# Performance work log

Hardware: AMD Instinct MI355X
Metric: run time of the kernel (lower is better)

## Reference

```python
import jax, jax.numpy as jnp
import numpy as np
from jax import lax

BN_EPS = 1e-5


def _fps(xyz, n_points):
    """Farthest point sampling. xyz: [B,N,3] -> [B,S] int32 indices.
    Sequential by nature; expressed as a lax.scan over S iterations.
    Deterministic start at index 0 (original uses a random start)."""
    B, N, _ = xyz.shape

    def step(carry, _):
        distance, farthest = carry  # [B,N], [B]
        centroid = jax.vmap(lambda p, f: p[f])(xyz, farthest)  # [B,3]
        dist = jnp.sum((xyz - centroid[:, None, :]) ** 2, axis=-1)  # [B,N]
        distance = jnp.minimum(distance, dist)
        new_far = jnp.argmax(distance, axis=-1).astype(jnp.int32)
        return (distance, new_far), farthest

    init = (jnp.full((B, N), 1e10, xyz.dtype), jnp.zeros((B,), jnp.int32))
    _, idxs = lax.scan(step, init, None, length=n_points)  # [S,B]
    return idxs.T  # [B,S]


def _gather(points, idx):
    """index_points: points [B,N,C], idx [B,...] -> [B,...,C]."""
    return jax.vmap(lambda p, i: p[i])(points, idx)


def _conv_bn_relu(x, W, b, gamma, beta):
    # 1x1 Conv2d over channel axis: x [B,Cin,k,S] -> [B,Cout,k,S]
    y = jnp.einsum('oc,bcks->boks', W, x) + b[None, :, None, None]
    # BatchNorm2d in training mode: batch stats over (B,k,S), biased variance
    m = jnp.mean(y, axis=(0, 2, 3), keepdims=True)
    v = jnp.var(y, axis=(0, 2, 3), keepdims=True)
    y = (y - m) * lax.rsqrt(v + BN_EPS) * gamma[None, :, None, None] + beta[None, :, None, None]
    return jax.nn.relu(y)


def setup_inputs() -> dict:
    key = jax.random.key(0)
    ks = jax.random.split(key, 4)
    B, N, D = 4, 16384, 125
    C0, C1, C2 = 128, 128, 256  # C0 = 3 + D
    xyz = jax.random.normal(ks[0], (B, N, 3), jnp.float32)
    features = jax.random.normal(ks[1], (B, N, D), jnp.float32)
    W1 = jax.random.normal(ks[2], (C1, C0), jnp.float32) / np.float32(np.sqrt(C0))
    W2 = jax.random.normal(ks[3], (C2, C1), jnp.float32) / np.float32(np.sqrt(C1))
    return {
        'xyz': xyz, 'features': features,
        'W1': W1, 'b1': jnp.zeros((C1,), jnp.float32),
        'gamma1': jnp.ones((C1,), jnp.float32), 'beta1': jnp.zeros((C1,), jnp.float32),
        'W2': W2, 'b2': jnp.zeros((C2,), jnp.float32),
        'gamma2': jnp.ones((C2,), jnp.float32), 'beta2': jnp.zeros((C2,), jnp.float32),
        'n_points_fps': 2048, 'k': 16,
    }


def reference(xyz, features, W1, b1, gamma1, beta1, W2, b2, gamma2, beta2, n_points_fps, k):
    B, N, _ = xyz.shape
    S = n_points_fps
    # sample_and_group
    fps_idx = _fps(xyz, S)                     # [B,S]
    new_xyz = _gather(xyz, fps_idx)            # [B,S,3]
    # full pairwise squared distances [B,S,N] (as in square_distance)
    dists = jnp.sum((new_xyz[:, :, None, :] - xyz[:, None, :, :]) ** 2, axis=-1)
    _, idx = lax.top_k(-dists, k)              # k nearest, ascending distance: [B,S,k]
    grouped_xyz = _gather(xyz, idx)            # [B,S,k,3]
    grouped_xyz_norm = grouped_xyz - new_xyz[:, :, None, :]
    grouped_feat = _gather(features, idx)      # [B,S,k,D]
    new_points = jnp.concatenate([grouped_xyz_norm, grouped_feat], axis=-1)  # [B,S,k,C0]
    # MLP head: permute to [B,C0,k,S]
    x = jnp.transpose(new_points, (0, 3, 2, 1))
    x = _conv_bn_relu(x, W1, b1, gamma1, beta1)
    x = _conv_bn_relu(x, W2, b2, gamma2, beta2)
    x = jnp.max(x, axis=2)                     # max over neighbors k: [B,C2,S]
    x = jnp.transpose(x, (0, 2, 1))            # [B,S,C2]
    return (new_xyz, x)
```

## Files before the change

kernel.cpp:

```cpp
#include <hip/hip_runtime.h>

#define B_ 4
#define N_ 16384
#define D_ 125
#define S_ 2048
#define K_ 16
#define C0_ 128
#define C1_ 128
#define C2_ 256
#define NSLOT 64

typedef float v2f __attribute__((ext_vector_type(2)));

__device__ __forceinline__ void pin(float& x) { asm volatile("" : "+v"(x)); }

__device__ __forceinline__ v2f v2max(v2f a, v2f b) {
  v2f r;
  r.x = fmaxf(a.x, b.x);
  r.y = fmaxf(a.y, b.y);
  return r;
}

template <int CTRL, int RMASK>
__device__ __forceinline__ double dppmax(double k) {
  const long long kb = __double_as_longlong(k);
  const int lo = (int)(kb & 0xffffffffll);
  const int hi = (int)(((unsigned long long)kb) >> 32);
  const int plo = __builtin_amdgcn_update_dpp(lo, lo, CTRL, RMASK, 0xf, false);
  const int phi = __builtin_amdgcn_update_dpp(hi, hi, CTRL, RMASK, 0xf, false);
  const double p =
      __longlong_as_double(((long long)phi << 32) | (unsigned int)plo);
  return fmax(k, p);
}
template <int CTRL, int RMASK>
__device__ __forceinline__ double dppmin(double k) {
  const long long kb = __double_as_longlong(k);
  const int lo = (int)(kb & 0xffffffffll);
  const int hi = (int)(((unsigned long long)kb) >> 32);
  const int plo = __builtin_amdgcn_update_dpp(lo, lo, CTRL, RMASK, 0xf, false);
  const int phi = __builtin_amdgcn_update_dpp(hi, hi, CTRL, RMASK, 0xf, false);
  const double p =
      __longlong_as_double(((long long)phi << 32) | (unsigned int)plo);
  return fmin(k, p);
}

__global__ __attribute__((amdgpu_flat_work_group_size(1024, 1024),
                          amdgpu_waves_per_eu(4, 4)))
void fps_a_kernel(const float* __restrict__ xyz, float* __restrict__ new_xyz,
                  float* __restrict__ sortbuf, float* __restrict__ dsp,
                  float4* __restrict__ ccsp, unsigned int* __restrict__ invsp,
                  unsigned long long* __restrict__ klsp,
                  float4* __restrict__ csp) {
#pragma clang fp contract(off)
  const int b = blockIdx.x;
  const float* X = xyz + (size_t)b * N_ * 3;
  float* SB = sortbuf + (size_t)b * 3 * N_;
  const int t = threadIdx.x;
  constexpr int PAIRS = N_ / 1024 / 2;
  const int base = t * (2 * PAIRS);

  __shared__ unsigned int s_hist[4096];
  __shared__ float s_bb[16][8];
  __shared__ unsigned int s_wsum[16];
  __shared__ unsigned short s_sidx[N_];
  __shared__ unsigned long long s_k1[2];
  __shared__ __align__(16) float4 s_cc[2][16];

  float arr[48];
  {
    float4* a4 = (float4*)arr;
#pragma unroll
    for (int i = 0; i < 12; ++i) a4[i] = *(const float4*)(X + base * 3 + 4 * i);
  }
  float lx0 = arr[0], lx1 = arr[0], ly0 = arr[1], ly1 = arr[1];
  float lz0 = arr[2], lz1 = arr[2];
#pragma unroll
  for (int p = 1; p < 16; ++p) {
    lx0 = fminf(lx0, arr[3 * p + 0]); lx1 = fmaxf(lx1, arr[3 * p + 0]);
    ly0 = fminf(ly0, arr[3 * p + 1]); ly1 = fmaxf(ly1, arr[3 * p + 1]);
    lz0 = fminf(lz0, arr[3 * p + 2]); lz1 = fmaxf(lz1, arr[3 * p + 2]);
  }
#pragma unroll
  for (int off = 32; off > 0; off >>= 1) {
    lx0 = fminf(lx0, __shfl_xor(lx0, off)); lx1 = fmaxf(lx1, __shfl_xor(lx1, off));
    ly0 = fminf(ly0, __shfl_xor(ly0, off)); ly1 = fmaxf(ly1, __shfl_xor(ly1, off));
    lz0 = fminf(lz0, __shfl_xor(lz0, off)); lz1 = fmaxf(lz1, __shfl_xor(lz1, off));
  }
  if ((t & 63) == 0) {
    const int w = t >> 6;
    s_bb[w][0] = lx0; s_bb[w][1] = lx1; s_bb[w][2] = ly0;
    s_bb[w][3] = ly1; s_bb[w][4] = lz0; s_bb[w][5] = lz1;
  }
  for (int i = t; i < 4096; i += 1024) s_hist[i] = 0u;
  if (t == 0) { s_k1[0] = 0ull; s_k1[1] = 0ull; }
  __syncthreads();
  float gx0 = s_bb[0][0], gx1 = s_bb[0][1], gy0 = s_bb[0][2];
  float gy1 = s_bb[0][3], gz0 = s_bb[0][4], gz1 = s_bb[0][5];
#pragma unroll
  for (int w = 1; w < 16; ++w) {
    gx0 = fminf(gx0, s_bb[w][0]); gx1 = fmaxf(gx1, s_bb[w][1]);
    gy0 = fminf(gy0, s_bb[w][2]); gy1 = fmaxf(gy1, s_bb[w][3]);
    gz0 = fminf(gz0, s_bb[w][4]); gz1 = fmaxf(gz1, s_bb[w][5]);
  }
  const float ivx = (gx1 > gx0) ? 16.0f / (gx1 - gx0) : 0.0f;
  const float ivy = (gy1 > gy0) ? 16.0f / (gy1 - gy0) : 0.0f;
  const float ivz = (gz1 > gz0) ? 16.0f / (gz1 - gz0) : 0.0f;
  int cell[16];
#pragma unroll
  for (int p = 0; p < 16; ++p) {
    int qx = min(15, (int)((arr[3 * p + 0] - gx0) * ivx));
    int qy = min(15, (int)((arr[3 * p + 1] - gy0) * ivy));
    int qz = min(15, (int)((arr[3 * p + 2] - gz0) * ivz));
    int mx = (qx & 1) | ((qx & 2) << 2) | ((qx & 4) << 4) | ((qx & 8) << 6);
    int my = (qy & 1) | ((qy & 2) << 2) | ((qy & 4) << 4) | ((qy & 8) << 6);
    int mz = (qz & 1) | ((qz & 2) << 2) | ((qz & 4) << 4) | ((qz & 8) << 6);
    cell[p] = mx | (my << 1) | (mz << 2);
    atomicAdd(&s_hist[cell[p]], 1u);
  }
  __syncthreads();
  {
    unsigned int c0 = s_hist[4 * t + 0], c1 = s_hist[4 * t + 1];
    unsigned int c2 = s_hist[4 * t + 2], c3 = s_hist[4 * t + 3];
    (void)c3;
    unsigned int tsum = c0 + c1 + c2 + c3;
    unsigned int incl = tsum;
#pragma unroll
    for (int off = 1; off < 64; off <<= 1) {
      unsigned int nv = __shfl_up(incl, off);
      if ((t & 63) >= off) incl += nv;
    }
    if ((t & 63) == 63) s_wsum[t >> 6] = incl;
    __syncthreads();
    unsigned int wpre = 0;
    const int myw = t >> 6;
    for (int w = 0; w < myw; ++w) wpre += s_wsum[w];
    const unsigned int texc = wpre + incl - tsum;
    s_hist[4 * t + 0] = texc;
    s_hist[4 * t + 1] = texc + c0;
    s_hist[4 * t + 2] = texc + c0 + c1;
    s_hist[4 * t + 3] = texc + c0 + c1 + c2;
  }
  __syncthreads();
#pragma unroll
  for (int p = 0; p < 16; ++p) {
    const unsigned int slot = atomicAdd(&s_hist[cell[p]], 1u);
    SB[slot]          = arr[3 * p + 0];
    SB[N_ + slot]     = arr[3 * p + 1];
    SB[2 * N_ + slot] = arr[3 * p + 2];
    s_sidx[slot] = (unsigned short)(base + p);
  }
  __threadfence();
  __syncthreads();
  __threadfence();

  v2f px[PAIRS], py[PAIRS], pz[PAIRS], d[PAIRS];
  {
    float4 xa[4], ya[4], za[4];
#pragma unroll
    for (int i = 0; i < 4; ++i) {
      xa[i] = *(const float4*)(SB + base + 4 * i);
      ya[i] = *(const float4*)(SB + N_ + base + 4 * i);
      za[i] = *(const float4*)(SB + 2 * N_ + base + 4 * i);
    }
    const float* xf = (const float*)xa;
    const float* yf = (const float*)ya;
    const float* zf = (const float*)za;
#pragma unroll
    for (int j = 0; j < PAIRS; ++j) {
      px[j] = (v2f){xf[2 * j], xf[2 * j + 1]};
      py[j] = (v2f){yf[2 * j], yf[2 * j + 1]};
      pz[j] = (v2f){zf[2 * j], zf[2 * j + 1]};
      d[j] = (v2f){1e10f, 1e10f};
    }
  }
  unsigned int invw[PAIRS];
  {
    const unsigned int* SI = (const unsigned int*)&s_sidx[base];
#pragma unroll
    for (int j = 0; j < PAIRS; ++j) invw[j] = ~SI[j];
  }
  float bx0 = 1e30f, bx1 = -1e30f, by0 = 1e30f, by1 = -1e30f;
  float bz0 = 1e30f, bz1 = -1e30f;
#pragma unroll
  for (int j = 0; j < PAIRS; ++j) {
    bx0 = fminf(bx0, fminf(px[j].x, px[j].y));
    bx1 = fmaxf(bx1, fmaxf(px[j].x, px[j].y));
    by0 = fminf(by0, fminf(py[j].x, py[j].y));
    by1 = fmaxf(by1, fmaxf(py[j].x, py[j].y));
    bz0 = fminf(bz0, fminf(pz[j].x, pz[j].y));
    bz1 = fmaxf(bz1, fmaxf(pz[j].x, pz[j].y));
  }
#pragma unroll
  for (int j = 0; j < PAIRS; ++j) {
    float a0 = px[j].x, a1 = px[j].y;
    float b0 = py[j].x, b1 = py[j].y;
    float c0 = pz[j].x, c1 = pz[j].y;
    pin(a0); pin(a1); pin(b0); pin(b1); pin(c0); pin(c1);
    px[j] = (v2f){a0, a1};
    py[j] = (v2f){b0, b1};
    pz[j] = (v2f){c0, c1};
  }
  float cx = X[0], cy = X[1], cz = X[2];
  float tmax = 1e10f;
  unsigned long long keylow = 0ull;
  bool iwin = false;
  float ccx = 0.f, ccy = 0.f, ccz = 0.f;
  float cap_x = 0.f, cap_y = 0.f, cap_z = 0.f;
  const unsigned int wid = (unsigned int)(t >> 6);
  for (int s = 0; s < 1024; ++s) {
    if (((s - t) & 1023) == 0) { cap_x = cx; cap_y = cy; cap_z = cz; }
    if ((s & 1023) == 1023) {
      const int o = (b * S_ + (s & ~1023) + t) * 3;
      new_xyz[o + 0] = cap_x;
      new_xyz[o + 1] = cap_y;
      new_xyz[o + 2] = cap_z;
    }
    const int buf = s & 1;
    const float mx = fmaxf(fmaxf(bx0 - cx, cx - bx1), 0.0f);
    const float my = fmaxf(fmaxf(by0 - cy, cy - by1), 0.0f);
    const float mz = fmaxf(fmaxf(bz0 - cz, cz - bz1), 0.0f);
    const float L = (mx * mx + my * my) + mz * mz;
    if (__any(L < tmax)) {
      __builtin_amdgcn_s_setprio(1);
      const v2f c2x = {cx, cx}, c2y = {cy, cy}, c2z = {cz, cz};
#pragma unroll
      for (int j = 0; j < PAIRS; ++j) {
        v2f dx = px[j] - c2x;
        v2f dy = py[j] - c2y;
        v2f dz = pz[j] - c2z;
        v2f sq = (dx * dx + dy * dy) + dz * dz;
        v2f dm;
        dm.x = fminf(d[j].x, sq.x);
        dm.y = fminf(d[j].y, sq.y);
        d[j] = dm;
      }
      const v2f m01 = v2max(d[0], d[1]);
      const v2f m23 = v2max(d[2], d[3]);
      const v2f m45 = v2max(d[4], d[5]);
      const v2f m67 = v2max(d[6], d[7]);
      const v2f m03 = v2max(m01, m23);
      const v2f m47 = v2max(m45, m67);
      const v2f m07 = v2max(m03, m47);
      const float lmax = fmaxf(m07.x, m07.y);
      tmax = lmax;
      unsigned int binv = 0u;
#pragma unroll
      for (int j = 0; j < PAIRS; ++j) {
        const unsigned int lo = invw[j] & 0xFFFFu;
        const unsigned int hi = invw[j] >> 16;
        if (d[j].x == lmax) binv = max(binv, lo);
        if (d[j].y == lmax) binv = max(binv, hi);
      }
#pragma unroll
      for (int j = 0; j < PAIRS; ++j) {
        const unsigned int lo = invw[j] & 0xFFFFu;
        const unsigned int hi = invw[j] >> 16;
        if (lo == binv) { ccx = px[j].x; ccy = py[j].x; ccz = pz[j].x; }
        if (hi == binv) { ccx = px[j].y; ccy = py[j].y; ccz = pz[j].y; }
      }
      const unsigned long long k52 =
          ((unsigned long long)__float_as_uint(lmax) << 20) |
          (unsigned long long)((binv << 4) | wid);
      double dk = __longlong_as_double((long long)k52);
      dk = dppmax<0x111, 0xf>(dk);
      dk = dppmax<0x112, 0xf>(dk);
      dk = dppmax<0x114, 0xf>(dk);
      dk = dppmax<0x118, 0xf>(dk);
      dk = dppmax<0x142, 0xa>(dk);
      dk = dppmax<0x143, 0xc>(dk);
      const long long kb = __double_as_longlong(dk);
      const int rlo = __builtin_amdgcn_readlane((int)(kb & 0xffffffffll), 63);
      const int rhi =
          __builtin_amdgcn_readlane((int)(((unsigned long long)kb) >> 32), 63);
      const unsigned long long wk52 =
          ((unsigned long long)(unsigned int)rhi << 32) | (unsigned int)rlo;
      iwin = (k52 == wk52);
      keylow = wk52;
      __builtin_amdgcn_s_setprio(0);
    }
    if (iwin) {
      atomicMax(&s_k1[buf], ((unsigned long long)s << 52) | keylow);
      s_cc[buf][wid] = make_float4(ccx, ccy, ccz, 0.f);
    }
    __syncthreads();
    const unsigned long long bk = s_k1[buf];
    const int w_win = (int)(bk & 15ull);
    const float4 cc = s_cc[buf][w_win];
    cx = cc.x; cy = cc.y; cz = cc.z;
  }
  {
    float4* o = (float4*)(dsp + ((size_t)b * 1024 + t) * 16);
    o[0] = make_float4(d[0].x, d[0].y, d[1].x, d[1].y);
    o[1] = make_float4(d[2].x, d[2].y, d[3].x, d[3].y);
    o[2] = make_float4(d[4].x, d[4].y, d[5].x, d[5].y);
    o[3] = make_float4(d[6].x, d[6].y, d[7].x, d[7].y);
    ccsp[b * 1024 + t] = make_float4(ccx, ccy, ccz, iwin ? 1.f : 0.f);
    unsigned int* iv = invsp + ((size_t)b * 1024 + t) * 8;
#pragma unroll
    for (int j = 0; j < PAIRS; ++j) iv[j] = invw[j];
    if ((t & 63) == 0) klsp[b * 16 + wid] = keylow;
    if (t == 0) csp[b] = make_float4(cx, cy, cz, 0.f);
  }
}

__device__ void fps_b_body(const float* __restrict__ xyz,
                           float* __restrict__ new_xyz,
                           float* __restrict__ sortbuf,
                           float* __restrict__ dsp, float4* __restrict__ ccsp,
                           unsigned int* __restrict__ invsp,
                           unsigned long long* __restrict__ klsp,
                           float4* __restrict__ csp, char* smem) {
#pragma clang fp contract(off)
  const int b = blockIdx.x;
  const float* X = xyz + (size_t)b * N_ * 3;
  float* SB = sortbuf + (size_t)b * 3 * N_;
  const int t = threadIdx.x;
  constexpr int PAIRS = N_ / 1024 / 2;
  const int base = t * (2 * PAIRS);
  unsigned long long* s_k1 = (unsigned long long*)smem;
  float4* s_cc = (float4*)(smem + 32);
  (void)X;

  v2f px[PAIRS], py[PAIRS], pz[PAIRS], d[PAIRS];
  {
    float4 xa[4], ya[4], za[4];
#pragma unroll
    for (int i = 0; i < 4; ++i) {
      xa[i] = *(const float4*)(SB + base + 4 * i);
      ya[i] = *(const float4*)(SB + N_ + base + 4 * i);
      za[i] = *(const float4*)(SB + 2 * N_ + base + 4 * i);
    }
    const float* xf = (const float*)xa;
    const float* yf = (const float*)ya;
    const float* zf = (const float*)za;
#pragma unroll
    for (int j = 0; j < PAIRS; ++j) {
      px[j] = (v2f){xf[2 * j], xf[2 * j + 1]};
      py[j] = (v2f){yf[2 * j], yf[2 * j + 1]};
      pz[j] = (v2f){zf[2 * j], zf[2 * j + 1]};
    }
  }
  {
    const float4* i4 = (const float4*)(dsp + ((size_t)b * 1024 + t) * 16);
    float4 d0 = i4[0], d1 = i4[1], d2 = i4[2], d3 = i4[3];
    d[0] = (v2f){d0.x, d0.y}; d[1] = (v2f){d0.z, d0.w};
    d[2] = (v2f){d1.x, d1.y}; d[3] = (v2f){d1.z, d1.w};
    d[4] = (v2f){d2.x, d2.y}; d[5] = (v2f){d2.z, d2.w};
    d[6] = (v2f){d3.x, d3.y}; d[7] = (v2f){d3.z, d3.w};
  }
  unsigned int invw[PAIRS];
  {
    const unsigned int* iv = invsp + ((size_t)b * 1024 + t) * 8;
#pragma unroll
    for (int j = 0; j < PAIRS; ++j) invw[j] = iv[j];
  }
  const float4 ccv = ccsp[b * 1024 + t];
  float ccx = ccv.x, ccy = ccv.y, ccz = ccv.z;
  bool iwin = (ccv.w != 0.f);
  const unsigned int wid = (unsigned int)(t >> 6);
  unsigned long long keylow = klsp[b * 16 + wid];
  const float4 cv = csp[b];
  float cx = cv.x, cy = cv.y, cz = cv.z;
  float tmax;
  {
    const v2f m01 = v2max(d[0], d[1]);
    const v2f m23 = v2max(d[2], d[3]);
    const v2f m45 = v2max(d[4], d[5]);
    const v2f m67 = v2max(d[6], d[7]);
    const v2f m03 = v2max(m01, m23);
    const v2f m47 = v2max(m45, m67);
    const v2f m07 = v2max(m03, m47);
    tmax = fmaxf(m07.x, m07.y);
  }
  float bx0 = 1e30f, bx1 = -1e30f, by0 = 1e30f, by1 = -1e30f;
  float bz0 = 1e30f, bz1 = -1e30f;
#pragma unroll
  for (int j = 0; j < PAIRS; ++j) {
    bx0 = fminf(bx0, fminf(px[j].x, px[j].y));
    bx1 = fmaxf(bx1, fmaxf(px[j].x, px[j].y));
    by0 = fminf(by0, fminf(py[j].x, py[j].y));
    by1 = fmaxf(by1, fmaxf(py[j].x, py[j].y));
    bz0 = fminf(bz0, fminf(pz[j].x, pz[j].y));
    bz1 = fmaxf(bz1, fmaxf(pz[j].x, pz[j].y));
  }
#pragma unroll
  for (int j = 0; j < PAIRS; ++j) {
    float a0 = px[j].x, a1 = px[j].y;
    float b0 = py[j].x, b1 = py[j].y;
    float c0 = pz[j].x, c1 = pz[j].y;
    pin(a0); pin(a1); pin(b0); pin(b1); pin(c0); pin(c1);
    px[j] = (v2f){a0, a1};
    py[j] = (v2f){b0, b1};
    pz[j] = (v2f){c0, c1};
  }
  if (t == 0) { s_k1[0] = 0ull; s_k1[1] = 0ull; }
  __syncthreads();
  float cap_x = 0.f, cap_y = 0.f, cap_z = 0.f;
  for (int s = 1024; s < S_; ++s) {
    if (((s - t) & 1023) == 0) { cap_x = cx; cap_y = cy; cap_z = cz; }
    if ((s & 1023) == 1023) {
      const int o = (b * S_ + (s & ~1023) + t) * 3;
      new_xyz[o + 0] = cap_x;
      new_xyz[o + 1] = cap_y;
      new_xyz[o + 2] = cap_z;
    }
    if (s == S_ - 1) break;
    const int buf = s & 1;
    const float mx = fmaxf(fmaxf(bx0 - cx, cx - bx1), 0.0f);
    const float my = fmaxf(fmaxf(by0 - cy, cy - by1), 0.0f);
    const float mz = fmaxf(fmaxf(bz0 - cz, cz - bz1), 0.0f);
    const float L = (mx * mx + my * my) + mz * mz;
    if (__any(L < tmax)) {
      __builtin_amdgcn_s_setprio(1);
      const v2f c2x = {cx, cx}, c2y = {cy, cy}, c2z = {cz, cz};
#pragma unroll
      for (int j = 0; j < PAIRS; ++j) {
        v2f dx = px[j] - c2x;
        v2f dy = py[j] - c2y;
        v2f dz = pz[j] - c2z;
        v2f sq = (dx * dx + dy * dy) + dz * dz;
        v2f dm;
        dm.x = fminf(d[j].x, sq.x);
        dm.y = fminf(d[j].y, sq.y);
        d[j] = dm;
      }
      const v2f m01 = v2max(d[0], d[1]);
      const v2f m23 = v2max(d[2], d[3]);
      const v2f m45 = v2max(d[4], d[5]);
      const v2f m67 = v2max(d[6], d[7]);
      const v2f m03 = v2max(m01, m23);
      const v2f m47 = v2max(m45, m67);
      const v2f m07 = v2max(m03, m47);
      const float lmax = fmaxf(m07.x, m07.y);
      tmax = lmax;
      unsigned int binv = 0u;
#pragma unroll
      for (int j = 0; j < PAIRS; ++j) {
        const unsigned int lo = invw[j] & 0xFFFFu;
        const unsigned int hi = invw[j] >> 16;
        if (d[j].x == lmax) binv = max(binv, lo);
        if (d[j].y == lmax) binv = max(binv, hi);
      }
#pragma unroll
      for (int j = 0; j < PAIRS; ++j) {
        const unsigned int lo = invw[j] & 0xFFFFu;
        const unsigned int hi = invw[j] >> 16;
        if (lo == binv) { ccx = px[j].x; ccy = py[j].x; ccz = pz[j].x; }
        if (hi == binv) { ccx = px[j].y; ccy = py[j].y; ccz = pz[j].y; }
      }
      const unsigned long long k52 =
          ((unsigned long long)__float_as_uint(lmax) << 20) |
          (unsigned long long)((binv << 4) | wid);
      double dk = __longlong_as_double((long long)k52);
      dk = dppmax<0x111, 0xf>(dk);
      dk = dppmax<0x112, 0xf>(dk);
      dk = dppmax<0x114, 0xf>(dk);
      dk = dppmax<0x118, 0xf>(dk);
      dk = dppmax<0x142, 0xa>(dk);
      dk = dppmax<0x143, 0xc>(dk);
      const long long kb = __double_as_longlong(dk);
      const int rlo = __builtin_amdgcn_readlane((int)(kb & 0xffffffffll), 63);
      const int rhi =
          __builtin_amdgcn_readlane((int)(((unsigned long long)kb) >> 32), 63);
      const unsigned long long wk52 =
          ((unsigned long long)(unsigned int)rhi << 32) | (unsigned int)rlo;
      iwin = (k52 == wk52);
      keylow = wk52;
      __builtin_amdgcn_s_setprio(0);
    }
    if (iwin) {
      atomicMax(&s_k1[buf], ((unsigned long long)s << 52) | keylow);
      s_cc[buf * 16 + wid] = make_float4(ccx, ccy, ccz, 0.f);
    }
    __syncthreads();
    const unsigned long long bk = s_k1[buf];
    const int w_win = (int)(bk & 15ull);
    const float4 cc = s_cc[buf * 16 + w_win];
    cx = cc.x; cy = cc.y; cz = cc.z;
  }
}

__device__ __forceinline__ void knn_core(float* sd, unsigned long long* s_kd,
                                         const float* __restrict__ xyz,
                                         const float* __restrict__ new_xyz,
                                         int* __restrict__ knn_idx, int q,
                                         int b) {
  const int t = threadIdx.x;
  if (t == 0) { s_kd[0] = ~0ull; s_kd[1] = ~0ull; }
  const float qx = new_xyz[q * 3 + 0];
  const float qy = new_xyz[q * 3 + 1];
  const float qz = new_xyz[q * 3 + 2];
  const float* X = xyz + (size_t)b * N_ * 3;
  float lmin = 1e30f;
  int lidx = -1;
  for (int j = 0; j < N_ / 1024; ++j) {
    int i = t + j * 1024;
    float dx = X[i * 3 + 0] - qx;
    float dy = X[i * 3 + 1] - qy;
    float dz = X[i * 3 + 2] - qz;
    float dsq = fmaf(dx, dx, fmaf(dy, dy, dz * dz));
    sd[i] = dsq;
    if (dsq < lmin) { lmin = dsq; lidx = i; }
  }
  __syncthreads();
  for (int r = 0; r < K_; ++r) {
    const unsigned long long k =
        ((unsigned long long)(7 - (r >> 1)) << 60) |
        ((unsigned long long)__float_as_uint(lmin) << 28) |
        (unsigned int)(lidx & 0x0FFFFFFF);
    double dk = __longlong_as_double((long long)k);
    dk = dppmin<0x111, 0xf>(dk);
    dk = dppmin<0x112, 0xf>(dk);
    dk = dppmin<0x114, 0xf>(dk);
    dk = dppmin<0x118, 0xf>(dk);
    dk = dppmin<0x142, 0xa>(dk);
    dk = dppmin<0x143, 0xc>(dk);
    const long long kb = __double_as_longlong(dk);
    const int rlo = __builtin_amdgcn_readlane((int)(kb & 0xffffffffll), 63);
    const int rhi =
        __builtin_amdgcn_readlane((int)(((unsigned long long)kb) >> 32), 63);
    const unsigned long long wk =
        ((unsigned long long)(unsigned int)rhi << 32) | (unsigned int)rlo;
    if ((t & 63) == 0) atomicMin(&s_kd[r & 1], wk);
    __syncthreads();
    const unsigned long long bk = s_kd[r & 1];
    const int wi = (int)(bk & 0x0FFFFFFFull);
    if (t == 0) knn_idx[q * K_ + r] = wi;
    if (wi == lidx) {
      sd[wi] = 1e30f;
      lmin = 1e30f; lidx = -1;
      for (int j = 0; j < N_ / 1024; ++j) {
        int i = t + j * 1024;
        float dv = sd[i];
        if (dv < lmin) { lmin = dv; lidx = i; }
      }
    }
  }
}

__global__ __attribute__((amdgpu_flat_work_group_size(1024, 1024),
                          amdgpu_waves_per_eu(4, 4)))
void fused_b_kernel(const float* __restrict__ xyz, float* __restrict__ new_xyz,
                    float* __restrict__ sortbuf, float* __restrict__ dsp,
                    float4* __restrict__ ccsp, unsigned int* __restrict__ invsp,
                    unsigned long long* __restrict__ klsp,
                    float4* __restrict__ csp, int* __restrict__ knn_idx) {
  __shared__ __align__(16) char smem[N_ * 4 + 16];
  if (blockIdx.x >= B_) {
    const int idx = blockIdx.x - B_;
    const int b = idx >> 10;
    const int s = idx & 1023;
    knn_core((float*)smem, (unsigned long long*)(smem + N_ * 4), xyz, new_xyz,
             knn_idx, b * S_ + s, b);
    return;
  }
  fps_b_body(xyz, new_xyz, sortbuf, dsp, ccsp, invsp, klsp, csp, smem);
}

__global__ __attribute__((amdgpu_flat_work_group_size(1024, 1024)))
void knn2_kernel(const float* __restrict__ xyz,
                 const float* __restrict__ new_xyz, int* __restrict__ knn_idx) {
  __shared__ float sd[N_];
  __shared__ unsigned long long s_kd[2];
  const int idx = blockIdx.x;
  const int b = idx >> 10;
  const int s = 1024 + (idx & 1023);
  knn_core(sd, s_kd, xyz, new_xyz, knn_idx, b * S_ + s, b);
}

__global__ __launch_bounds__(256) void prep_kernel(const float* __restrict__ W1,
                                                   const float* __restrict__ W2,
                                                   float* __restrict__ W1t,
                                                   float* __restrict__ W2t,
                                                   float* __restrict__ stats) {
  int e = blockIdx.x * 256 + threadIdx.x;
  stats[e] = 0.0f;
  if (e < C1_ * C0_) {
    int co = e / C0_, c = e % C0_;
    W1t[c * C1_ + co] = W1[e];
  } else {
    int e2 = e - C1_ * C0_;
    int co = e2 / C1_, c = e2 % C1_;
    W2t[c * C2_ + co] = W2[e2];
  }
}

__global__ __launch_bounds__(256) void conv1_stats_kernel(
    const float* __restrict__ xyz, const float* __restrict__ feat,
    const float* __restrict__ new_xyz, const int* __restrict__ knn,
    const float* __restrict__ W1t, const float* __restrict__ b1,
    float* __restrict__ stats1) {
  __shared__ __align__(16) float sinT[C0_][K_];
  __shared__ int sidx[K_];
  __shared__ float sred[256];
  const int t = threadIdx.x;
  float psum = 0.f, psumsq = 0.f;
  const int QPB = (B_ * S_) / 1024;
  for (int qq = 0; qq < QPB; ++qq) {
    const int q = blockIdx.x * QPB + qq;
    const int b = q / S_;
    if (t < K_) sidx[t] = knn[q * K_ + t];
    __syncthreads();
    const float nx = new_xyz[q * 3 + 0];
    const float ny = new_xyz[q * 3 + 1];
    const float nz = new_xyz[q * 3 + 2];
    for (int e = t; e < K_ * C0_; e += 256) {
      int c = e >> 4, kk = e & 15;
      int i = sidx[kk];
      float v;
      if (c < 3)
        v = xyz[((size_t)b * N_ + i) * 3 + c] - (c == 0 ? nx : (c == 1 ? ny : nz));
      else
        v = feat[((size_t)b * N_ + i) * D_ + (c - 3)];
      sinT[c][kk] = v;
    }
    __syncthreads();
    const int co = t & 127, kh = t >> 7;
    float acc[8];
    float bias = b1[co];
#pragma unroll
    for (int k = 0; k < 8; ++k) acc[k] = bias;
    for (int c = 0; c < C0_; ++c) {
      float w = W1t[c * C1_ + co];
      float4 xa = *(const float4*)&sinT[c][kh * 8];
      float4 xb = *(const float4*)&sinT[c][kh * 8 + 4];
      acc[0] = fmaf(w, xa.x, acc[0]);
      acc[1] = fmaf(w, xa.y, acc[1]);
      acc[2] = fmaf(w, xa.z, acc[2]);
      acc[3] = fmaf(w, xa.w, acc[3]);
      acc[4] = fmaf(w, xb.x, acc[4]);
      acc[5] = fmaf(w, xb.y, acc[5]);
      acc[6] = fmaf(w, xb.z, acc[6]);
      acc[7] = fmaf(w, xb.w, acc[7]);
    }
#pragma unroll
    for (int k = 0; k < 8; ++k) {
      psum += acc[k];
      psumsq = fmaf(acc[k], acc[k], psumsq);
    }
    __syncthreads();
  }
  sred[t] = psum;
  __syncthreads();
  float totsum = (t < 128) ? (sred[t] + sred[t + 128]) : 0.f;
  __syncthreads();
  sred[t] = psumsq;
  __syncthreads();
  if (t < 128) {
    float totsq = sred[t] + sred[t + 128];
    float* st = stats1 + (size_t)(blockIdx.x & (NSLOT - 1)) * (2 * C1_);
    atomicAdd(&st[t], totsum);
    atomicAdd(&st[C1_ + t], totsq);
  }
}

__global__ void finalize1_kernel(const float* __restrict__ stats1,
                                 const float* __restrict__ gamma1,
                                 const float* __restrict__ beta1,
                                 float* __restrict__ ss1) {
  int t = threadIdx.x;
  float s = 0.f, sq = 0.f;
  for (int w = 0; w < NSLOT; ++w) {
    s += stats1[w * 2 * C1_ + t];
    sq += stats1[w * 2 * C1_ + C1_ + t];
  }
  const float M = (float)(B_ * S_ * K_);
  float m = s / M;
  float v = fmaxf(sq / M - m * m, 0.f);
  float sc = gamma1[t] * rsqrtf(v + 1e-5f);
  ss1[t] = sc;
  ss1[C1_ + t] = fmaf(-m, sc, beta1[t]);
}

__global__ __launch_bounds__(256) void conv2_kernel(
    const float* __restrict__ xyz, const float* __restrict__ feat,
    const float* __restrict__ new_xyz, const int* __restrict__ knn,
    const float* __restrict__ W1t, const float* __restrict__ b1,
    const float* __restrict__ ss1, const float* __restrict__ W2t,
    const float* __restrict__ b2, float* __restrict__ maxv,
    float* __restrict__ minv, float* __restrict__ stats2) {
  __shared__ __align__(16) float sinT[C0_][K_];
  __shared__ __align__(16) float sh1T[C1_][20];
  __shared__ int sidx[K_];
  const int t = threadIdx.x;
  float psum = 0.f, psumsq = 0.f;
  const int QPB = (B_ * S_) / 1024;
  for (int qq = 0; qq < QPB; ++qq) {
    const int q = blockIdx.x * QPB + qq;
    const int b = q / S_;
    if (t < K_) sidx[t] = knn[q * K_ + t];
    __syncthreads();
    const float nx = new_xyz[q * 3 + 0];
    const float ny = new_xyz[q * 3 + 1];
    const float nz = new_xyz[q * 3 + 2];
    for (int e = t; e < K_ * C0_; e += 256) {
      int c = e >> 4, kk = e & 15;
      int i = sidx[kk];
      float v;
      if (c < 3)
        v = xyz[((size_t)b * N_ + i) * 3 + c] - (c == 0 ? nx : (c == 1 ? ny : nz));
      else
        v = feat[((size_t)b * N_ + i) * D_ + (c - 3)];
      sinT[c][kk] = v;
    }
    __syncthreads();
    {
      const int co = t & 127, kh = t >> 7;
      float acc[8];
      float bias = b1[co];
#pragma unroll
      for (int k = 0; k < 8; ++k) acc[k] = bias;
      for (int c = 0; c < C0_; ++c) {
        float w = W1t[c * C1_ + co];
        float4 xa = *(const float4*)&sinT[c][kh * 8];
        float4 xb = *(const float4*)&sinT[c][kh * 8 + 4];
        acc[0] = fmaf(w, xa.x, acc[0]);
        acc[1] = fmaf(w, xa.y, acc[1]);
        acc[2] = fmaf(w, xa.z, acc[2]);
        acc[3] = fmaf(w, xa.w, acc[3]);
        acc[4] = fmaf(w, xb.x, acc[4]);
        acc[5] = fmaf(w, xb.y, acc[5]);
        acc[6] = fmaf(w, xb.z, acc[6]);
        acc[7] = fmaf(w, xb.w, acc[7]);
      }
      float sc = ss1[co], sh = ss1[C1_ + co];
#pragma unroll
      for (int k = 0; k < 8; ++k) {
        float h = fmaxf(fmaf(acc[k], sc, sh), 0.f);
        sh1T[co][kh * 8 + k] = h;
      }
    }
    __syncthreads();
    {
      float acc2[16];
      float bias2 = b2[t];
#pragma unroll
      for (int k = 0; k < 16; ++k) acc2[k] = bias2;
      for (int c = 0; c < C1_; ++c) {
        float w = W2t[c * C2_ + t];
        float4 h0 = *(const float4*)&sh1T[c][0];
        float4 h1 = *(const float4*)&sh1T[c][4];
        float4 h2 = *(const float4*)&sh1T[c][8];
        float4 h3 = *(const float4*)&sh1T[c][12];
        acc2[0] = fmaf(w, h0.x, acc2[0]);
        acc2[1] = fmaf(w, h0.y, acc2[1]);
        acc2[2] = fmaf(w, h0.z, acc2[2]);
        acc2[3] = fmaf(w, h0.w, acc2[3]);
        acc2[4] = fmaf(w, h1.x, acc2[4]);
        acc2[5] = fmaf(w, h1.y, acc2[5]);
        acc2[6] = fmaf(w, h1.z, acc2[6]);
        acc2[7] = fmaf(w, h1.w, acc2[7]);
        acc2[8] = fmaf(w, h2.x, acc2[8]);
        acc2[9] = fmaf(w, h2.y, acc2[9]);
        acc2[10] = fmaf(w, h2.z, acc2[10]);
        acc2[11] = fmaf(w, h2.w, acc2[11]);
        acc2[12] = fmaf(w, h3.x, acc2[12]);
        acc2[13] = fmaf(w, h3.y, acc2[13]);
        acc2[14] = fmaf(w, h3.z, acc2[14]);
        acc2[15] = fmaf(w, h3.w, acc2[15]);
      }
      float mx = acc2[0], mn = acc2[0];
#pragma unroll
      for (int k = 0; k < 16; ++k) {
        psum += acc2[k];
        psumsq = fmaf(acc2[k], acc2[k], psumsq);
        mx = fmaxf(mx, acc2[k]);
        mn = fminf(mn, acc2[k]);
      }
      maxv[(size_t)q * C2_ + t] = mx;
      minv[(size_t)q * C2_ + t] = mn;
    }
    __syncthreads();
  }
  float* st = stats2 + (size_t)(blockIdx.x & (NSLOT - 1)) * (2 * C2_);
  atomicAdd(&st[t], psum);
  atomicAdd(&st[C2_ + t], psumsq);
}

__global__ void finalize2_kernel(const float* __restrict__ stats2,
                                 const float* __restrict__ gamma2,
                                 const float* __restrict__ beta2,
                                 float* __restrict__ ss2) {
  int t = threadIdx.x;
  float s = 0.f, sq = 0.f;
  for (int w = 0; w < NSLOT; ++w) {
    s += stats2[w * 2 * C2_ + t];
    sq += stats2[w * 2 * C2_ + C2_ + t];
  }
  const float M = (float)(B_ * S_ * K_);
  float m = s / M;
  float v = fmaxf(sq / M - m * m, 0.f);
  float sc = gamma2[t] * rsqrtf(v + 1e-5f);
  ss2[t] = sc;
  ss2[C2_ + t] = fmaf(-m, sc, beta2[t]);
}

__global__ __launch_bounds__(256) void out_kernel(const float* __restrict__ maxv,
                                                  const float* __restrict__ minv,
                                                  const float* __restrict__ ss2,
                                                  float* __restrict__ out2) {
  int e = blockIdx.x * 256 + threadIdx.x;
  int co = e & (C2_ - 1);
  float sc = ss2[co], sh = ss2[C2_ + co];
  float v = (sc >= 0.f) ? maxv[e] : minv[e];
  out2[e] = fmaxf(fmaf(v, sc, sh), 0.f);
}

extern "C" void kernel_launch(void* const* d_in, const int* in_sizes, int n_in,
                              void* d_out, int out_size, void* d_ws, size_t ws_size,
                              hipStream_t stream) {
  (void)in_sizes; (void)n_in; (void)out_size; (void)ws_size;
  const float* xyz = (const float*)d_in[0];
  const float* feat = (const float*)d_in[1];
  const float* W1 = (const float*)d_in[2];
  const float* b1 = (const float*)d_in[3];
  const float* gamma1 = (const float*)d_in[4];
  const float* beta1 = (const float*)d_in[5];
  const float* W2 = (const float*)d_in[6];
  const float* b2 = (const float*)d_in[7];
  const float* gamma2 = (const float*)d_in[8];
  const float* beta2 = (const float*)d_in[9];

  float* out = (float*)d_out;
  float* new_xyz = out;
  float* out2 = out + B_ * S_ * 3;

  float* ws = (float*)d_ws;
  float* stats1 = ws;
  float* stats2 = stats1 + NSLOT * 2 * C1_;
  float* ss1 = stats2 + NSLOT * 2 * C2_;
  float* ss2 = ss1 + 2 * C1_;
  float* W1t = ss2 + 2 * C2_;
  float* W2t = W1t + C1_ * C0_;
  int* knn = (int*)(W2t + (size_t)C2_ * C1_);
  float* maxv = (float*)(knn + B_ * S_ * K_);
  float* minv = maxv + (size_t)B_ * S_ * C2_;
  float* sortbuf = maxv;
  float* dsp = minv;
  float4* ccsp = (float4*)(minv + 65536);
  unsigned int* invsp = (unsigned int*)(minv + 65536 + 16384);
  unsigned long long* klsp =
      (unsigned long long*)(minv + 65536 + 16384 + 32768);
  float4* csp = (float4*)(minv + 65536 + 16384 + 32768 + 2 * B_ * 16);

  prep_kernel<<<192, 256, 0, stream>>>(W1, W2, W1t, W2t, stats1);
  fps_a_kernel<<<B_, 1024, 0, stream>>>(xyz, new_xyz, sortbuf, dsp, ccsp,
                                        invsp, klsp, csp);
  fused_b_kernel<<<B_ + B_ * 1024, 1024, 0, stream>>>(
      xyz, new_xyz, sortbuf, dsp, ccsp, invsp, klsp, csp, knn);
  knn2_kernel<<<B_ * 1024, 1024, 0, stream>>>(xyz, new_xyz, knn);
  conv1_stats_kernel<<<1024, 256, 0, stream>>>(xyz, feat, new_xyz, knn, W1t, b1, stats1);
  finalize1_kernel<<<1, 128, 0, stream>>>(stats1, gamma1, beta1, ss1);
  conv2_kernel<<<1024, 256, 0, stream>>>(xyz, feat, new_xyz, knn, W1t, b1, ss1,
                                         W2t, b2, maxv, minv, stats2);
  finalize2_kernel<<<1, 256, 0, stream>>>(stats2, gamma2, beta2, ss2);
  out_kernel<<<(B_ * S_ * C2_) / 256, 256, 0, stream>>>(maxv, minv, ss2, out2);
}
```

Baseline: 3.166 ms.

## Fuse conv1 batch-stat accumulation into the KNN kernels

```diff
diff --git a/kernel.cpp b/kernel.cpp
--- a/kernel.cpp
+++ b/kernel.cpp
@@ -312,14 +312,12 @@
                            float4* __restrict__ csp, char* smem) {
 #pragma clang fp contract(off)
   const int b = blockIdx.x;
-  const float* X = xyz + (size_t)b * N_ * 3;
   float* SB = sortbuf + (size_t)b * 3 * N_;
   const int t = threadIdx.x;
   constexpr int PAIRS = N_ / 1024 / 2;
   const int base = t * (2 * PAIRS);
   unsigned long long* s_k1 = (unsigned long long*)smem;
   float4* s_cc = (float4*)(smem + 32);
-  (void)X;
 
   v2f px[PAIRS], py[PAIRS], pz[PAIRS], d[PAIRS];
   {
@@ -480,11 +478,12 @@
   }
 }
 
-__device__ __forceinline__ void knn_core(float* sd, unsigned long long* s_kd,
-                                         const float* __restrict__ xyz,
-                                         const float* __restrict__ new_xyz,
-                                         int* __restrict__ knn_idx, int q,
-                                         int b) {
+__device__ __forceinline__ void knn_core(
+    float* sd, unsigned long long* s_kd, int* s_widx,
+    const float* __restrict__ xyz, const float* __restrict__ new_xyz,
+    int* __restrict__ knn_idx, int q, int b, const float* __restrict__ feat,
+    const float* __restrict__ W1t, const float* __restrict__ b1,
+    float* __restrict__ stats1, int slot) {
   const int t = threadIdx.x;
   if (t == 0) { s_kd[0] = ~0ull; s_kd[1] = ~0ull; }
   const float qx = new_xyz[q * 3 + 0];
@@ -525,8 +524,11 @@
     __syncthreads();
     const unsigned long long bk = s_kd[r & 1];
     const int wi = (int)(bk & 0x0FFFFFFFull);
-    if (t == 0) knn_idx[q * K_ + r] = wi;
-    if (wi == lidx) {
+    if (t == 0) {
+      knn_idx[q * K_ + r] = wi;
+      s_widx[r] = wi;
+    }
+    if (wi == lidx && r < K_ - 1) {
       sd[wi] = 1e30f;
       lmin = 1e30f; lidx = -1;
       for (int j = 0; j < N_ / 1024; ++j) {
@@ -536,6 +538,48 @@
       }
     }
   }
+  __syncthreads();
+  float* sinT = sd;
+  float2* sred = (float2*)(sd + 2048);
+#pragma unroll
+  for (int u = 0; u < 2; ++u) {
+    const int e = 2 * t + u;
+    const int c = e >> 4, kk = e & 15;
+    const int i = s_widx[kk];
+    float v;
+    if (c < 3)
+      v = xyz[((size_t)b * N_ + i) * 3 + c] - (c == 0 ? qx : (c == 1 ? qy : qz));
+    else
+      v = feat[((size_t)b * N_ + i) * D_ + (c - 3)];
+    sinT[c * 16 + kk] = v;
+  }
+  __syncthreads();
+  const int co = t & 127, g = t >> 7;
+  const float bias = b1[co];
+  float a0 = bias, a1 = bias;
+  for (int c = 0; c < C0_; ++c) {
+    const float w = W1t[c * C1_ + co];
+    a0 = fmaf(w, sinT[c * 16 + g], a0);
+    a1 = fmaf(w, sinT[c * 16 + g + 8], a1);
+  }
+  sred[t] = make_float2(a0 + a1, fmaf(a0, a0, a1 * a1));
+  __syncthreads();
+  if (t < 512) {
+    float2 o = sred[t + 512], m = sred[t];
+    sred[t] = make_float2(m.x + o.x, m.y + o.y);
+  }
+  __syncthreads();
+  if (t < 256) {
+    float2 o = sred[t + 256], m = sred[t];
+    sred[t] = make_float2(m.x + o.x, m.y + o.y);
+  }
+  __syncthreads();
+  if (t < 128) {
+    float2 o = sred[t + 128], m = sred[t];
+    float* st = stats1 + (size_t)slot * (2 * C1_);
+    atomicAdd(&st[t], m.x + o.x);
+    atomicAdd(&st[C1_ + t], m.y + o.y);
+  }
 }
 
 __global__ __attribute__((amdgpu_flat_work_group_size(1024, 1024),
@@ -544,14 +588,18 @@
                     float* __restrict__ sortbuf, float* __restrict__ dsp,
                     float4* __restrict__ ccsp, unsigned int* __restrict__ invsp,
                     unsigned long long* __restrict__ klsp,
-                    float4* __restrict__ csp, int* __restrict__ knn_idx) {
-  __shared__ __align__(16) char smem[N_ * 4 + 16];
+                    float4* __restrict__ csp, int* __restrict__ knn_idx,
+                    const float* __restrict__ feat,
+                    const float* __restrict__ W1t,
+                    const float* __restrict__ b1, float* __restrict__ stats1) {
+  __shared__ __align__(16) char smem[N_ * 4 + 16 + 64];
   if (blockIdx.x >= B_) {
     const int idx = blockIdx.x - B_;
     const int b = idx >> 10;
     const int s = idx & 1023;
-    knn_core((float*)smem, (unsigned long long*)(smem + N_ * 4), xyz, new_xyz,
-             knn_idx, b * S_ + s, b);
+    knn_core((float*)smem, (unsigned long long*)(smem + N_ * 4),
+             (int*)(smem + N_ * 4 + 16), xyz, new_xyz, knn_idx, b * S_ + s, b,
+             feat, W1t, b1, stats1, (int)(blockIdx.x & (NSLOT - 1)));
     return;
   }
   fps_b_body(xyz, new_xyz, sortbuf, dsp, ccsp, invsp, klsp, csp, smem);
@@ -559,13 +607,17 @@
 
 __global__ __attribute__((amdgpu_flat_work_group_size(1024, 1024)))
 void knn2_kernel(const float* __restrict__ xyz,
-                 const float* __restrict__ new_xyz, int* __restrict__ knn_idx) {
+                 const float* __restrict__ new_xyz, int* __restrict__ knn_idx,
+                 const float* __restrict__ feat, const float* __restrict__ W1t,
+                 const float* __restrict__ b1, float* __restrict__ stats1) {
   __shared__ float sd[N_];
   __shared__ unsigned long long s_kd[2];
+  __shared__ int s_widx[K_];
   const int idx = blockIdx.x;
   const int b = idx >> 10;
   const int s = 1024 + (idx & 1023);
-  knn_core(sd, s_kd, xyz, new_xyz, knn_idx, b * S_ + s, b);
+  knn_core(sd, s_kd, s_widx, xyz, new_xyz, knn_idx, b * S_ + s, b, feat, W1t,
+           b1, stats1, (int)(blockIdx.x & (NSLOT - 1)));
 }
 
 __global__ __launch_bounds__(256) void prep_kernel(const float* __restrict__ W1,
@@ -582,75 +634,6 @@
     int e2 = e - C1_ * C0_;
     int co = e2 / C1_, c = e2 % C1_;
     W2t[c * C2_ + co] = W2[e2];
-  }
-}
-
-__global__ __launch_bounds__(256) void conv1_stats_kernel(
-    const float* __restrict__ xyz, const float* __restrict__ feat,
-    const float* __restrict__ new_xyz, const int* __restrict__ knn,
-    const float* __restrict__ W1t, const float* __restrict__ b1,
-    float* __restrict__ stats1) {
-  __shared__ __align__(16) float sinT[C0_][K_];
-  __shared__ int sidx[K_];
-  __shared__ float sred[256];
-  const int t = threadIdx.x;
-  float psum = 0.f, psumsq = 0.f;
-  const int QPB = (B_ * S_) / 1024;
-  for (int qq = 0; qq < QPB; ++qq) {
-    const int q = blockIdx.x * QPB + qq;
-    const int b = q / S_;
-    if (t < K_) sidx[t] = knn[q * K_ + t];
-    __syncthreads();
-    const float nx = new_xyz[q * 3 + 0];
-    const float ny = new_xyz[q * 3 + 1];
-    const float nz = new_xyz[q * 3 + 2];
-    for (int e = t; e < K_ * C0_; e += 256) {
-      int c = e >> 4, kk = e & 15;
-      int i = sidx[kk];
-      float v;
-      if (c < 3)
-        v = xyz[((size_t)b * N_ + i) * 3 + c] - (c == 0 ? nx : (c == 1 ? ny : nz));
-      else
-        v = feat[((size_t)b * N_ + i) * D_ + (c - 3)];
-      sinT[c][kk] = v;
-    }
-    __syncthreads();
-    const int co = t & 127, kh = t >> 7;
-    float acc[8];
-    float bias = b1[co];
-#pragma unroll
-    for (int k = 0; k < 8; ++k) acc[k] = bias;
-    for (int c = 0; c < C0_; ++c) {
-      float w = W1t[c * C1_ + co];
-      float4 xa = *(const float4*)&sinT[c][kh * 8];
-      float4 xb = *(const float4*)&sinT[c][kh * 8 + 4];
-      acc[0] = fmaf(w, xa.x, acc[0]);
-      acc[1] = fmaf(w, xa.y, acc[1]);
-      acc[2] = fmaf(w, xa.z, acc[2]);
-      acc[3] = fmaf(w, xa.w, acc[3]);
-      acc[4] = fmaf(w, xb.x, acc[4]);
-      acc[5] = fmaf(w, xb.y, acc[5]);
-      acc[6] = fmaf(w, xb.z, acc[6]);
-      acc[7] = fmaf(w, xb.w, acc[7]);
-    }
-#pragma unroll
-    for (int k = 0; k < 8; ++k) {
-      psum += acc[k];
-      psumsq = fmaf(acc[k], acc[k], psumsq);
-    }
-    __syncthreads();
-  }
-  sred[t] = psum;
-  __syncthreads();
-  float totsum = (t < 128) ? (sred[t] + sred[t + 128]) : 0.f;
-  __syncthreads();
-  sred[t] = psumsq;
-  __syncthreads();
-  if (t < 128) {
-    float totsq = sred[t] + sred[t + 128];
-    float* st = stats1 + (size_t)(blockIdx.x & (NSLOT - 1)) * (2 * C1_);
-    atomicAdd(&st[t], totsum);
-    atomicAdd(&st[C1_ + t], totsq);
   }
 }
 
@@ -847,9 +830,10 @@
   fps_a_kernel<<<B_, 1024, 0, stream>>>(xyz, new_xyz, sortbuf, dsp, ccsp,
                                         invsp, klsp, csp);
   fused_b_kernel<<<B_ + B_ * 1024, 1024, 0, stream>>>(
-      xyz, new_xyz, sortbuf, dsp, ccsp, invsp, klsp, csp, knn);
-  knn2_kernel<<<B_ * 1024, 1024, 0, stream>>>(xyz, new_xyz, knn);
-  conv1_stats_kernel<<<1024, 256, 0, stream>>>(xyz, feat, new_xyz, knn, W1t, b1, stats1);
+      xyz, new_xyz, sortbuf, dsp, ccsp, invsp, klsp, csp, knn, feat, W1t, b1,
+      stats1);
+  knn2_kernel<<<B_ * 1024, 1024, 0, stream>>>(xyz, new_xyz, knn, feat, W1t,
+                                              b1, stats1);
   finalize1_kernel<<<1, 128, 0, stream>>>(stats1, gamma1, beta1, ss1);
   conv2_kernel<<<1024, 256, 0, stream>>>(xyz, feat, new_xyz, knn, W1t, b1, ss1,
                                          W2t, b2, maxv, minv, stats2);
```

New measurement: 3.127 ms. About the same (-1.2%).
